# Performance work log

Measured on AMD Instinct MI355X. Metric: run time of the kernel, lower is better.

The kernel has to match this reference:

```python
import math
import jax, jax.numpy as jnp
import numpy as np

B, T, H, A, F = 2, 2048, 2048, 2048, 8192
L, LID, EPS = 24, 0, 1e-5
NEG_INF = -1e38


def setup_inputs() -> dict:
    key = jax.random.key(0)
    ks = jax.random.split(key, 8)
    s = 0.02
    # RWKV init-derived time parameters for layer_id=0, num_hidden_layers=24
    ratio_0_to_1 = LID / (L - 1)          # 0.0
    ratio_1_to_almost_0 = 1.0 - LID / L    # 1.0
    x = jnp.arange(H, dtype=jnp.float32) / H
    tmk = jnp.power(x, ratio_1_to_almost_0)
    tmv = tmk + 0.3 * ratio_0_to_1
    tmr = jnp.power(x, 0.5 * ratio_1_to_almost_0)
    zigzag = 0.5 * (jnp.arange(1, A + 1, dtype=jnp.float32) % 3 - 1)
    time_first = jnp.full((A,), math.log(0.3), dtype=jnp.float32) + zigzag
    h = jnp.arange(A, dtype=jnp.float32)
    time_decay = -5.0 + 8.0 * (h / (A - 1)) ** (0.7 + 1.3 * ratio_0_to_1)
    return {
        'hidden': jax.random.normal(ks[0], (B, T, H), jnp.float32),
        'pre_w': jnp.ones((H,), jnp.float32), 'pre_b': jnp.zeros((H,), jnp.float32),
        'ln1_w': jnp.ones((H,), jnp.float32), 'ln1_b': jnp.zeros((H,), jnp.float32),
        'ln2_w': jnp.ones((H,), jnp.float32), 'ln2_b': jnp.zeros((H,), jnp.float32),
        'time_decay': time_decay, 'time_first': time_first,
        'tmk': tmk, 'tmv': tmv, 'tmr': tmr,
        'Wk': jax.random.normal(ks[1], (H, A), jnp.float32) * s,
        'Wv': jax.random.normal(ks[2], (H, A), jnp.float32) * s,
        'Wr': jax.random.normal(ks[3], (H, A), jnp.float32) * s,
        'Wo': jax.random.normal(ks[4], (A, H), jnp.float32) * s,
        'f_tmk': jnp.power(x, ratio_1_to_almost_0), 'f_tmr': jnp.power(x, ratio_1_to_almost_0),
        'f_Wk': jax.random.normal(ks[5], (H, F), jnp.float32) * s,
        'f_Wr': jax.random.normal(ks[6], (H, H), jnp.float32) * s,
        'f_Wv': jax.random.normal(ks[7], (F, H), jnp.float32) * s,
    }


def _ln(x, w, b):
    mu = x.mean(-1, keepdims=True)
    var = ((x - mu) ** 2).mean(-1, keepdims=True)
    return (x - mu) * jax.lax.rsqrt(var + EPS) * w + b


def _token_shift(x):
    # sx state is zeros at init: prepend a zero row, drop the last token
    return jnp.concatenate((jnp.zeros_like(x[:, :1, :]), x[:, :-1, :]), axis=1)


def _forward(hidden, pre_w, pre_b, ln1_w, ln1_b, ln2_w, ln2_b,
             time_decay, time_first, tmk, tmv, tmr, Wk, Wv, Wr, Wo,
             f_tmk, f_tmr, f_Wk, f_Wr, f_Wv):
    h0 = _ln(hidden, pre_w, pre_b)          # pre_ln (layer_id == 0)
    # ---- time mixing (RwkvSelfAttention) ----
    x1 = _ln(h0, ln1_w, ln1_b)
    cx = _token_shift(x1)
    kx = x1 * tmk + cx * (1 - tmk)
    vx = x1 * tmv + cx * (1 - tmv)
    rx = x1 * tmr + cx * (1 - tmr)
    r = jax.nn.sigmoid(rx @ Wr)             # [B,T,A]
    k = kx @ Wk
    v = vx @ Wv
    w_decay = -jnp.exp(time_decay)          # [A]

    def step(carry, kv):
        aa, bb, pp = carry                  # each [B,A]
        kk, vv = kv                         # each [B,A]
        ww = time_first + kk
        q = jnp.maximum(pp, ww)
        e1 = jnp.exp(pp - q)
        e2 = jnp.exp(ww - q)
        out = (e1 * aa + e2 * vv) / (e1 * bb + e2)
        ww2 = w_decay + pp
        q2 = jnp.maximum(ww2, kk)
        e1 = jnp.exp(ww2 - q2)
        e2 = jnp.exp(kk - q2)
        return (e1 * aa + e2 * vv, e1 * bb + e2, q2), out

    init = (jnp.zeros((B, A), k.dtype), jnp.zeros((B, A), k.dtype),
            jnp.full((B, A), NEG_INF, jnp.float32))
    _, wkv = jax.lax.scan(step, init, (jnp.swapaxes(k, 0, 1), jnp.swapaxes(v, 0, 1)))
    wkv = jnp.swapaxes(wkv, 0, 1)           # [B,T,A]
    h1 = h0 + (r * wkv) @ Wo
    # ---- channel mixing (RwkvFeedForward) ----
    x2 = _ln(h1, ln2_w, ln2_b)
    cx2 = _token_shift(x2)
    kx2 = x2 * f_tmk + cx2 * (1 - f_tmk)
    rx2 = x2 * f_tmr + cx2 * (1 - f_tmr)
    r2 = jax.nn.sigmoid(rx2 @ f_Wr)
    kk2 = jnp.square(jax.nn.relu(kx2 @ f_Wk))
    return h1 + r2 * (kk2 @ f_Wv)


def reference(hidden, pre_w, pre_b, ln1_w, ln1_b, ln2_w, ln2_b,
              time_decay, time_first, tmk, tmv, tmr, Wk, Wv, Wr, Wo,
              f_tmk, f_tmr, f_Wk, f_Wr, f_Wv):
    return _forward(hidden, pre_w, pre_b, ln1_w, ln1_b, ln2_w, ln2_b,
                    time_decay, time_first, tmk, tmv, tmr, Wk, Wv, Wr, Wo,
                    f_tmk, f_tmr, f_Wk, f_Wr, f_Wv)
```

## Files before the change

### kernel.cpp

```cpp
#include <hip/hip_runtime.h>

#define B_  2
#define T_  2048
#define H_  2048
#define A_  2048
#define F_  8192
#define BT_ 4096

typedef __bf16  bf16x8 __attribute__((ext_vector_type(8)));
typedef float   f32x4  __attribute__((ext_vector_type(4)));
typedef short   short8 __attribute__((ext_vector_type(8)));

__device__ __forceinline__ float bf2f(unsigned short b) {
  return __uint_as_float(((unsigned)b) << 16);
}
__device__ __forceinline__ unsigned short f2bf(float f) {
  unsigned u = __float_as_uint(f);
  unsigned r = (u + 0x7FFFu + ((u >> 16) & 1u)) >> 16;
  return (unsigned short)r;
}

typedef __attribute__((address_space(3))) void lds_void_t;
typedef __attribute__((address_space(1))) const void gc_void_t;
__device__ __forceinline__ void gload_lds16(const void* g, void* l) {
  __builtin_amdgcn_global_load_lds((gc_void_t*)g, (lds_void_t*)l, 16, 0, 0);
}

__global__ void canary_kernel(float* out) { out[threadIdx.x] = 1000.0f; }

__global__ __launch_bounds__(256) void transpose5_kernel(
    const float* __restrict__ s0, const float* __restrict__ s1,
    const float* __restrict__ s2, const float* __restrict__ s3,
    const float* __restrict__ s4, unsigned short* __restrict__ dstbase)
{
  __shared__ float tile[32][33];
  const int z = blockIdx.z;
  const float* src = (z == 0) ? s0 : (z == 1) ? s1 : (z == 2) ? s2 : (z == 3) ? s3 : s4;
  unsigned short* dst = dstbase + (size_t)z * 2048 * 2048;
  const int tx = threadIdx.x & 31;
  const int ty = threadIdx.x >> 5;
  const int n0 = blockIdx.x * 32;
  const int k0 = blockIdx.y * 32;
#pragma unroll
  for (int i = 0; i < 32; i += 8)
    tile[ty + i][tx] = src[(size_t)(k0 + ty + i) * 2048 + n0 + tx];
  __syncthreads();
#pragma unroll
  for (int i = 0; i < 32; i += 8)
    dst[(size_t)(n0 + ty + i) * 2048 + k0 + tx] = f2bf(tile[tx][ty + i]);
}

__global__ __launch_bounds__(256) void transpose_bf16_kernel(
    const float* __restrict__ src, unsigned short* __restrict__ dst, int Kd, int Nd)
{
  __shared__ float tile[32][33];
  const int tx = threadIdx.x & 31;
  const int ty = threadIdx.x >> 5;
  const int n0 = blockIdx.x * 32;
  const int k0 = blockIdx.y * 32;
#pragma unroll
  for (int i = 0; i < 32; i += 8)
    tile[ty + i][tx] = src[(size_t)(k0 + ty + i) * Nd + n0 + tx];
  __syncthreads();
#pragma unroll
  for (int i = 0; i < 32; i += 8)
    dst[(size_t)(n0 + ty + i) * Kd + k0 + tx] = f2bf(tile[tx][ty + i]);
}

__device__ __forceinline__ void block_reduce2(float& a, float& b) {
#pragma unroll
  for (int off = 32; off > 0; off >>= 1) {
    a += __shfl_down(a, off, 64);
    b += __shfl_down(b, off, 64);
  }
  __shared__ float sa[4], sb[4];
  const int lane = threadIdx.x & 63, w = threadIdx.x >> 6;
  __syncthreads();
  if (lane == 0) { sa[w] = a; sb[w] = b; }
  __syncthreads();
  a = sa[0] + sa[1] + sa[2] + sa[3];
  b = sb[0] + sb[1] + sb[2] + sb[3];
}

__global__ __launch_bounds__(256) void ln_pre_kernel(
    const float* __restrict__ hidden,
    const float* __restrict__ pw, const float* __restrict__ pb,
    const float* __restrict__ w1, const float* __restrict__ b1,
    float* __restrict__ h0, unsigned short* __restrict__ x1)
{
  const int row = blockIdx.x, tid = threadIdx.x;
  const int c0 = tid * 8;
  const size_t base = (size_t)row * H_ + c0;
  float x[8];
  float4 v0 = *(const float4*)(hidden + base);
  float4 v1 = *(const float4*)(hidden + base + 4);
  x[0]=v0.x; x[1]=v0.y; x[2]=v0.z; x[3]=v0.w;
  x[4]=v1.x; x[5]=v1.y; x[6]=v1.z; x[7]=v1.w;
  float s = 0.f, s2 = 0.f;
#pragma unroll
  for (int j = 0; j < 8; ++j) { s += x[j]; s2 += x[j]*x[j]; }
  block_reduce2(s, s2);
  float mu  = s * (1.f / H_);
  float inv = rsqrtf(fmaxf(s2 * (1.f / H_) - mu*mu, 0.f) + 1e-5f);
  float y[8];
#pragma unroll
  for (int j = 0; j < 8; ++j) y[j] = (x[j] - mu) * inv * pw[c0+j] + pb[c0+j];
  *(float4*)(h0 + base)     = make_float4(y[0],y[1],y[2],y[3]);
  *(float4*)(h0 + base + 4) = make_float4(y[4],y[5],y[6],y[7]);
  s = 0.f; s2 = 0.f;
#pragma unroll
  for (int j = 0; j < 8; ++j) { s += y[j]; s2 += y[j]*y[j]; }
  block_reduce2(s, s2);
  mu  = s * (1.f / H_);
  inv = rsqrtf(fmaxf(s2 * (1.f / H_) - mu*mu, 0.f) + 1e-5f);
  unsigned o[4];
#pragma unroll
  for (int p = 0; p < 4; ++p) {
    unsigned lo = f2bf((y[2*p]   - mu) * inv * w1[c0+2*p]   + b1[c0+2*p]);
    unsigned hi = f2bf((y[2*p+1] - mu) * inv * w1[c0+2*p+1] + b1[c0+2*p+1]);
    o[p] = lo | (hi << 16);
  }
  *(uint4*)(x1 + base) = make_uint4(o[0], o[1], o[2], o[3]);
}

__global__ __launch_bounds__(256) void lnmix2_kernel(
    const float* __restrict__ h1,
    const float* __restrict__ w_, const float* __restrict__ b_,
    const float* __restrict__ tmk_, const float* __restrict__ tmr_,
    unsigned short* __restrict__ kx2b, unsigned short* __restrict__ rx2b)
{
  const int row = blockIdx.x, tid = threadIdx.x;
  const int t = row & (T_ - 1);
  const int c0 = tid * 8;
  const size_t base = (size_t)row * H_ + c0;
  float x[8], p[8];
  {
    float4 v0 = *(const float4*)(h1 + base);
    float4 v1 = *(const float4*)(h1 + base + 4);
    x[0]=v0.x; x[1]=v0.y; x[2]=v0.z; x[3]=v0.w;
    x[4]=v1.x; x[5]=v1.y; x[6]=v1.z; x[7]=v1.w;
  }
  const bool hasp = (t > 0);
  if (hasp) {
    float4 v0 = *(const float4*)(h1 + base - H_);
    float4 v1 = *(const float4*)(h1 + base - H_ + 4);
    p[0]=v0.x; p[1]=v0.y; p[2]=v0.z; p[3]=v0.w;
    p[4]=v1.x; p[5]=v1.y; p[6]=v1.z; p[7]=v1.w;
  } else {
#pragma unroll
    for (int j = 0; j < 8; ++j) p[j] = 0.f;
  }
  float s = 0.f, s2 = 0.f;
#pragma unroll
  for (int j = 0; j < 8; ++j) { s += x[j]; s2 += x[j]*x[j]; }
  block_reduce2(s, s2);
  const float mu  = s * (1.f / H_);
  const float inv = rsqrtf(fmaxf(s2 * (1.f / H_) - mu*mu, 0.f) + 1e-5f);
  float sp = 0.f, sp2 = 0.f;
#pragma unroll
  for (int j = 0; j < 8; ++j) { sp += p[j]; sp2 += p[j]*p[j]; }
  block_reduce2(sp, sp2);
  const float mup  = sp * (1.f / H_);
  const float invp = rsqrtf(fmaxf(sp2 * (1.f / H_) - mup*mup, 0.f) + 1e-5f);
  unsigned ok[4], orr[4];
#pragma unroll
  for (int q = 0; q < 4; ++q) {
    unsigned ko = 0, ro = 0;
#pragma unroll
    for (int h = 0; h < 2; ++h) {
      const int j = q*2 + h;
      const float xr = (x[j] - mu) * inv * w_[c0+j] + b_[c0+j];
      const float cr = hasp ? (p[j] - mup) * invp * w_[c0+j] + b_[c0+j] : 0.f;
      ko |= (unsigned)f2bf(fmaf(xr - cr, tmk_[c0+j], cr)) << (h*16);
      ro |= (unsigned)f2bf(fmaf(xr - cr, tmr_[c0+j], cr)) << (h*16);
    }
    ok[q] = ko; orr[q] = ro;
  }
  *(uint4*)(kx2b + base) = make_uint4(ok[0],ok[1],ok[2],ok[3]);
  *(uint4*)(rx2b + base) = make_uint4(orr[0],orr[1],orr[2],orr[3]);
}

__global__ __launch_bounds__(256) void mix3_kernel(
    const unsigned short* __restrict__ x,
    const float* __restrict__ mk_, const float* __restrict__ mv_, const float* __restrict__ mr_,
    unsigned short* __restrict__ kx, unsigned short* __restrict__ vx, unsigned short* __restrict__ rx)
{
  const int row = blockIdx.x;
  const int t = row & (T_ - 1);
  const int c0 = threadIdx.x * 8;
  const size_t base = (size_t)row * H_ + c0;
  uint4 xv = *(const uint4*)(x + base);
  uint4 cv = make_uint4(0u,0u,0u,0u);
  if (t > 0) cv = *(const uint4*)(x + base - H_);
  const unsigned xs[4] = {xv.x, xv.y, xv.z, xv.w};
  const unsigned cs[4] = {cv.x, cv.y, cv.z, cv.w};
  unsigned ok[4], ov[4], orr[4];
#pragma unroll
  for (int p = 0; p < 4; ++p) {
    unsigned ko=0, vo=0, ro=0;
#pragma unroll
    for (int h = 0; h < 2; ++h) {
      const int j = p*2 + h;
      float xf = bf2f((unsigned short)((xs[p] >> (h*16)) & 0xFFFFu));
      float cf = bf2f((unsigned short)((cs[p] >> (h*16)) & 0xFFFFu));
      float d  = xf - cf;
      ko |= (unsigned)f2bf(fmaf(d, mk_[c0+j], cf)) << (h*16);
      vo |= (unsigned)f2bf(fmaf(d, mv_[c0+j], cf)) << (h*16);
      ro |= (unsigned)f2bf(fmaf(d, mr_[c0+j], cf)) << (h*16);
    }
    ok[p]=ko; ov[p]=vo; orr[p]=ro;
  }
  *(uint4*)(kx + base) = make_uint4(ok[0],ok[1],ok[2],ok[3]);
  *(uint4*)(vx + base) = make_uint4(ov[0],ov[1],ov[2],ov[3]);
  *(uint4*)(rx + base) = make_uint4(orr[0],orr[1],orr[2],orr[3]);
}

#define WKV_G 32
#define WKV_C 32
#define WKV_L 64

__global__ __launch_bounds__(1024) void wkv_scan_kernel(
    const unsigned short* __restrict__ kg, const unsigned short* __restrict__ vg,
    const unsigned short* __restrict__ rg,
    const float* __restrict__ time_first, const float* __restrict__ time_decay,
    unsigned short* __restrict__ rwkv)
{
  const int tid = threadIdx.x;
  const int al  = tid & (WKV_G - 1);
  const int c   = tid >> 5;
  const int b   = blockIdx.x >> 6;
  const int ag  = blockIdx.x & 63;
  const int a   = ag * WKV_G + al;
  const float tf = time_first[a];
  const float w  = -__expf(time_decay[a]);
  const size_t cb = (size_t)b * T_ * A_ + a + (size_t)c * WKV_L * A_;

  float aa = 0.f, bb = 0.f, pp = -1e38f;
  {
    float kb[4], vb[4];
#pragma unroll
    for (int j = 0; j < 4; ++j) {
      kb[j] = bf2f(kg[cb + (size_t)j * A_]);
      vb[j] = bf2f(vg[cb + (size_t)j * A_]);
    }
    for (int t0 = 0; t0 < WKV_L; t0 += 4) {
#pragma unroll
      for (int j = 0; j < 4; ++j) {
        const float kk = kb[j], vv = vb[j];
        const int tn = t0 + j + 4;
        if (tn < WKV_L) {
          kb[j] = bf2f(kg[cb + (size_t)tn * A_]);
          vb[j] = bf2f(vg[cb + (size_t)tn * A_]);
        }
        float ww2 = w + pp;
        float q2  = fmaxf(ww2, kk);
        float e1  = __expf(ww2 - q2);
        float e2  = __expf(kk  - q2);
        aa = e1*aa + e2*vv;
        bb = e1*bb + e2;
        pp = q2;
      }
    }
  }
  __shared__ float saa[WKV_C][WKV_G], sbb[WKV_C][WKV_G], spp[WKV_C][WKV_G];
  saa[c][al] = aa; sbb[c][al] = bb; spp[c][al] = pp;
  __syncthreads();

  if (tid < WKV_G) {
    float Aa = 0.f, Bb = 0.f, Pp = -1e38f;
    const float Lw = (float)WKV_L * w;
    for (int cc = 0; cc < WKV_C; ++cc) {
      const float na = saa[cc][tid], nb = sbb[cc][tid], np = spp[cc][tid];
      saa[cc][tid] = Aa; sbb[cc][tid] = Bb; spp[cc][tid] = Pp;
      const float p1 = Pp + Lw;
      const float pc = fmaxf(p1, np);
      const float f1 = __expf(p1 - pc);
      const float f2 = __expf(np - pc);
      Aa = f1*Aa + f2*na;
      Bb = f1*Bb + f2*nb;
      Pp = pc;
    }
  }
  __syncthreads();
  aa = saa[c][al]; bb = sbb[c][al]; pp = spp[c][al];

  {
    float kb[4], vb[4], rb[4];
#pragma unroll
    for (int j = 0; j < 4; ++j) {
      kb[j] = bf2f(kg[cb + (size_t)j * A_]);
      vb[j] = bf2f(vg[cb + (size_t)j * A_]);
      rb[j] = bf2f(rg[cb + (size_t)j * A_]);
    }
    for (int t0 = 0; t0 < WKV_L; t0 += 4) {
#pragma unroll
      for (int j = 0; j < 4; ++j) {
        const float kk = kb[j], vv = vb[j], rr = rb[j];
        const int tn = t0 + j + 4;
        if (tn < WKV_L) {
          kb[j] = bf2f(kg[cb + (size_t)tn * A_]);
          vb[j] = bf2f(vg[cb + (size_t)tn * A_]);
          rb[j] = bf2f(rg[cb + (size_t)tn * A_]);
        }
        float ww = tf + kk;
        float q  = fmaxf(pp, ww);
        float e1 = __expf(pp - q);
        float e2 = __expf(ww - q);
        float o  = (e1*aa + e2*vv) / (e1*bb + e2);
        float sr = 1.f / (1.f + __expf(-rr));
        rwkv[cb + (size_t)(t0 + j) * A_] = f2bf(sr * o);
        float ww2 = w + pp;
        float q2  = fmaxf(ww2, kk);
        e1 = __expf(ww2 - q2);
        e2 = __expf(kk  - q2);
        aa = e1*aa + e2*vv;
        bb = e1*bb + e2;
        pp = q2;
      }
    }
  }
}

enum { EPI_BF16 = 0, EPI_ADDIP = 1, EPI_RELU2 = 2, EPI_SIGADD = 3 };

template <int BM, int NBUF, int RG, int CG, int EPI>
__global__ __launch_bounds__(512) void gemm4_kernel(
    const unsigned short* __restrict__ Ap, const unsigned short* __restrict__ Bp,
    void* __restrict__ Cp, int K, int Nn,
    const unsigned short* __restrict__ sigb,
    size_t azB, size_t bzB, size_t czB)
{
  constexpr int BN = 256;
  constexpr int FM = BM / 32;
  constexpr int FN = 4;
  __shared__ unsigned short As[NBUF * BM * 64];
  __shared__ unsigned short Bs[NBUF * BN * 64];
  const int zz = blockIdx.z;
  Ap = (const unsigned short*)((const char*)Ap + zz * azB);
  Bp = (const unsigned short*)((const char*)Bp + zz * bzB);
  Cp = (void*)((char*)Cp + zz * czB);
  const int tid  = threadIdx.x;
  const int lane = tid & 63;
  const int lr = lane & 15;
  const int hi = lane >> 4;
  const int rx7 = lr & 7;
  const int wid = tid >> 6;
  const int wm = wid >> 2, wn = wid & 3;
  const int rowW = wm * (BM / 2);
  const int colW = wn * 64;
  const int gx = gridDim.x;
  const int gy = gridDim.y;
  const int flat = blockIdx.y * gx + blockIdx.x;
  const int xcd = flat & 7;
  const int j = flat >> 3;
  const int rgc = gy / RG;
  const int r_idx = xcd % rgc;
  const int c_idx = xcd / rgc;
  const int row_l = j % RG;
  const int col_l = j / RG;
  const long row0 = (long)(r_idx * RG + row_l) * BM;
  const long col0 = (long)(c_idx * CG + col_l) * BN;
  const unsigned short* Ab = Ap + (size_t)row0 * K;
  const unsigned short* Bb = Bp + (size_t)col0 * K;
  const int srow8 = tid >> 3;
  const int sslot = (tid & 7) ^ (srow8 & 7);
  f32x4 acc[FM][FN] = {};

  auto SP0 = [&](int bufi, int tt) {
    unsigned short* asb = As + bufi * (BM * 64);
    unsigned short* bsb = Bs + bufi * (BN * 64);
    const size_t ko = (size_t)tt * 64 + sslot * 8;
    gload_lds16(Ab + (size_t)srow8        * K + ko, asb + tid * 8);
    gload_lds16(Ab + (size_t)(srow8 + 64) * K + ko, asb + 4096 + tid * 8);
    gload_lds16(Bb + (size_t)srow8        * K + ko, bsb + tid * 8);
  };
  auto SP1 = [&](int bufi, int tt) {
    unsigned short* bsb = Bs + bufi * (BN * 64);
    const size_t ko = (size_t)tt * 64 + sslot * 8;
    gload_lds16(Bb + (size_t)(srow8 + 64)  * K + ko, bsb + 4096  + tid * 8);
    gload_lds16(Bb + (size_t)(srow8 + 128) * K + ko, bsb + 8192  + tid * 8);
    gload_lds16(Bb + (size_t)(srow8 + 192) * K + ko, bsb + 12288 + tid * 8);
  };
  auto SPq = [&](int bufi, int tt, int q) {
    const size_t ko = (size_t)tt * 64 + sslot * 8;
    if (q < 2) {
      unsigned short* asb = As + bufi * (BM * 64);
      gload_lds16(Ab + (size_t)(srow8 + q*128)      * K + ko, asb + q*8192 + tid * 8);
      gload_lds16(Ab + (size_t)(srow8 + q*128 + 64) * K + ko, asb + q*8192 + 4096 + tid * 8);
    } else {
      const int qq = q - 2;
      unsigned short* bsb = Bs + bufi * (BN * 64);
      gload_lds16(Bb + (size_t)(srow8 + qq*128)      * K + ko, bsb + qq*8192 + tid * 8);
      gload_lds16(Bb + (size_t)(srow8 + qq*128 + 64) * K + ko, bsb + qq*8192 + 4096 + tid * 8);
    }
  };

  const int nt = K >> 6;
  if constexpr (BM == 128) {
    SP0(0, 0); SP1(0, 0);
    if constexpr (NBUF == 3) { SP0(1, 1); SP1(1, 1); }
  } else {
#pragma unroll
    for (int q = 0; q < 4; ++q) SPq(0, 0, q);
  }
  int cur = 0;
  for (int t = 0; t < nt; ++t) {
    if constexpr (NBUF == 3) {
      if (t + 1 < nt) asm volatile("s_waitcnt vmcnt(6)" ::: "memory");
      else            asm volatile("s_waitcnt vmcnt(0)" ::: "memory");
    } else {
      asm volatile("s_waitcnt vmcnt(0)" ::: "memory");
    }
    __builtin_amdgcn_s_barrier();
    int nb = cur + (NBUF - 1); if (nb >= NBUF) nb -= NBUF;
    const unsigned short* asb = As + cur * (BM * 64);
    const unsigned short* bsb = Bs + cur * (BN * 64);
    if constexpr (BM == 128) {
      bf16x8 af0[4], bf0[4], af1[4], bf1[4];
      const int p0 = (0*4 + hi) ^ rx7;
      const int p1 = (1*4 + hi) ^ rx7;
#pragma unroll
      for (int m = 0; m < 4; ++m)
        af0[m] = __builtin_bit_cast(bf16x8,
            *(const short8*)(asb + (rowW + m*16 + lr) * 64 + p0*8));
#pragma unroll
      for (int n = 0; n < 4; ++n)
        bf0[n] = __builtin_bit_cast(bf16x8,
            *(const short8*)(bsb + (colW + n*16 + lr) * 64 + p0*8));
#pragma unroll
      for (int m = 0; m < 4; ++m)
        af1[m] = __builtin_bit_cast(bf16x8,
            *(const short8*)(asb + (rowW + m*16 + lr) * 64 + p1*8));
#pragma unroll
      for (int n = 0; n < 4; ++n)
        bf1[n] = __builtin_bit_cast(bf16x8,
            *(const short8*)(bsb + (colW + n*16 + lr) * 64 + p1*8));
      if (t + NBUF - 1 < nt) SP0(nb, t + NBUF - 1);
      asm volatile("s_waitcnt lgkmcnt(8)" ::: "memory");
      __builtin_amdgcn_sched_barrier(0);
      __builtin_amdgcn_s_setprio(1);
#pragma unroll
      for (int m = 0; m < 4; ++m)
#pragma unroll
        for (int n = 0; n < 4; ++n)
          acc[m][n] = __builtin_amdgcn_mfma_f32_16x16x32_bf16(af0[m], bf0[n], acc[m][n], 0, 0, 0);
      __builtin_amdgcn_s_setprio(0);
      if (t + NBUF - 1 < nt) SP1(nb, t + NBUF - 1);
      asm volatile("s_waitcnt lgkmcnt(0)" ::: "memory");
      __builtin_amdgcn_sched_barrier(0);
      __builtin_amdgcn_s_setprio(1);
#pragma unroll
      for (int m = 0; m < 4; ++m)
#pragma unroll
        for (int n = 0; n < 4; ++n)
          acc[m][n] = __builtin_amdgcn_mfma_f32_16x16x32_bf16(af1[m], bf1[n], acc[m][n], 0, 0, 0);
      __builtin_amdgcn_s_setprio(0);
    } else {
      bf16x8 aF[2][4], bF[2][4];
      const int p0 = (0*4 + hi) ^ rx7;
      const int p1 = (1*4 + hi) ^ rx7;
#pragma unroll
      for (int n = 0; n < 4; ++n)
        bF[0][n] = __builtin_bit_cast(bf16x8,
            *(const short8*)(bsb + (colW + n*16 + lr) * 64 + p0*8));
#pragma unroll
      for (int m = 0; m < 4; ++m)
        aF[0][m] = __builtin_bit_cast(bf16x8,
            *(const short8*)(asb + (rowW + m*16 + lr) * 64 + p0*8));
#pragma unroll
      for (int m = 0; m < 4; ++m)
        aF[1][m] = __builtin_bit_cast(bf16x8,
            *(const short8*)(asb + (rowW + (4+m)*16 + lr) * 64 + p0*8));
      if (t + 1 < nt) SPq(nb, t + 1, 0);
      asm volatile("s_waitcnt lgkmcnt(4)" ::: "memory");
      __builtin_amdgcn_sched_barrier(0);
      __builtin_amdgcn_s_setprio(1);
#pragma unroll
      for (int m = 0; m < 4; ++m)
#pragma unroll
        for (int n = 0; n < 4; ++n)
          acc[m][n] = __builtin_amdgcn_mfma_f32_16x16x32_bf16(aF[0][m], bF[0][n], acc[m][n], 0, 0, 0);
      __builtin_amdgcn_s_setprio(0);
#pragma unroll
      for (int n = 0; n < 4; ++n)
        bF[1][n] = __builtin_bit_cast(bf16x8,
            *(const short8*)(bsb + (colW + n*16 + lr) * 64 + p1*8));
#pragma unroll
      for (int m = 0; m < 4; ++m)
        aF[0][m] = __builtin_bit_cast(bf16x8,
            *(const short8*)(asb + (rowW + m*16 + lr) * 64 + p1*8));
      if (t + 1 < nt) SPq(nb, t + 1, 1);
      asm volatile("s_waitcnt lgkmcnt(8)" ::: "memory");
      __builtin_amdgcn_sched_barrier(0);
      __builtin_amdgcn_s_setprio(1);
#pragma unroll
      for (int m = 0; m < 4; ++m)
#pragma unroll
        for (int n = 0; n < 4; ++n)
          acc[4+m][n] = __builtin_amdgcn_mfma_f32_16x16x32_bf16(aF[1][m], bF[0][n], acc[4+m][n], 0, 0, 0);
      __builtin_amdgcn_s_setprio(0);
#pragma unroll
      for (int m = 0; m < 4; ++m)
        aF[1][m] = __builtin_bit_cast(bf16x8,
            *(const short8*)(asb + (rowW + (4+m)*16 + lr) * 64 + p1*8));
      if (t + 1 < nt) SPq(nb, t + 1, 2);
      asm volatile("s_waitcnt lgkmcnt(4)" ::: "memory");
      __builtin_amdgcn_sched_barrier(0);
      __builtin_amdgcn_s_setprio(1);
#pragma unroll
      for (int m = 0; m < 4; ++m)
#pragma unroll
        for (int n = 0; n < 4; ++n)
          acc[m][n] = __builtin_amdgcn_mfma_f32_16x16x32_bf16(aF[0][m], bF[1][n], acc[m][n], 0, 0, 0);
      __builtin_amdgcn_s_setprio(0);
      if (t + 1 < nt) SPq(nb, t + 1, 3);
      asm volatile("s_waitcnt lgkmcnt(0)" ::: "memory");
      __builtin_amdgcn_sched_barrier(0);
      __builtin_amdgcn_s_setprio(1);
#pragma unroll
      for (int m = 0; m < 4; ++m)
#pragma unroll
        for (int n = 0; n < 4; ++n)
          acc[4+m][n] = __builtin_amdgcn_mfma_f32_16x16x32_bf16(aF[1][m], bF[1][n], acc[4+m][n], 0, 0, 0);
      __builtin_amdgcn_s_setprio(0);
    }
    cur = (cur + 1 == NBUF) ? 0 : cur + 1;
  }

#pragma unroll
  for (int m = 0; m < FM; ++m) {
#pragma unroll
    for (int n = 0; n < FN; ++n) {
      const long col = col0 + colW + n*16 + lr;
#pragma unroll
      for (int j2 = 0; j2 < 4; ++j2) {
        const long row = row0 + rowW + m*16 + hi*4 + j2;
        const size_t idx = (size_t)row * Nn + col;
        const float v = acc[m][n][j2];
        if (EPI == EPI_BF16) {
          ((unsigned short*)Cp)[idx] = f2bf(v);
        } else if (EPI == EPI_ADDIP) {
          float* C = (float*)Cp;
          C[idx] = C[idx] + v;
        } else if (EPI == EPI_RELU2) {
          float rr = v > 0.f ? v : 0.f;
          ((unsigned short*)Cp)[idx] = f2bf(rr * rr);
        } else {
          float s = 1.f / (1.f + __expf(-bf2f(sigb[idx])));
          float* C = (float*)Cp;
          C[idx] = C[idx] + s * v;
        }
      }
    }
  }
}

#define MB(x) ((size_t)(x) << 20)
#define WS_NEED MB(184)

extern "C" void kernel_launch(void* const* d_in, const int* in_sizes, int n_in,
                              void* d_out, int out_size, void* d_ws, size_t ws_size,
                              hipStream_t stream) {
  const float* hidden     = (const float*)d_in[0];
  const float* pre_w      = (const float*)d_in[1];
  const float* pre_b      = (const float*)d_in[2];
  const float* ln1_w      = (const float*)d_in[3];
  const float* ln1_b      = (const float*)d_in[4];
  const float* ln2_w      = (const float*)d_in[5];
  const float* ln2_b      = (const float*)d_in[6];
  const float* time_decay = (const float*)d_in[7];
  const float* time_first = (const float*)d_in[8];
  const float* tmk        = (const float*)d_in[9];
  const float* tmv        = (const float*)d_in[10];
  const float* tmr        = (const float*)d_in[11];
  const float* Wk         = (const float*)d_in[12];
  const float* Wv         = (const float*)d_in[13];
  const float* Wr         = (const float*)d_in[14];
  const float* Wo         = (const float*)d_in[15];
  const float* f_tmk      = (const float*)d_in[16];
  const float* f_tmr      = (const float*)d_in[17];
  const float* f_Wk       = (const float*)d_in[18];
  const float* f_Wr       = (const float*)d_in[19];
  const float* f_Wv       = (const float*)d_in[20];
  float* out = (float*)d_out;
  char*  ws  = (char*)d_ws;

  if (ws_size < WS_NEED) {
    canary_kernel<<<1, 256, 0, stream>>>(out);
    return;
  }

  unsigned short* MX   = (unsigned short*)(ws + MB(0));
  unsigned short* fWkT = (unsigned short*)(ws + MB(0));
  unsigned short* fWvT = (unsigned short*)(ws + MB(32));
  unsigned short* WkT  = (unsigned short*)(ws + MB(64));
  unsigned short* WoT  = (unsigned short*)(ws + MB(88));
  unsigned short* fWrT = (unsigned short*)(ws + MB(96));
  unsigned short* KK   = (unsigned short*)(ws + MB(64));
  unsigned short* S1   = (unsigned short*)(ws + MB(104));
  unsigned short* kbuf = (unsigned short*)(ws + MB(120));
  unsigned short* vbuf = (unsigned short*)(ws + MB(136));
  unsigned short* rbuf = (unsigned short*)(ws + MB(152));
  unsigned short* M1   = (unsigned short*)(ws + MB(168));

  const dim3 blk(256);
  const dim3 blk512(512);
  const dim3 gSmall(8, 32);
  const dim3 gSmall3(8, 32, 3);
  const dim3 gRelu(32, 16);

  transpose5_kernel<<<dim3(64, 64, 5), blk, 0, stream>>>(Wk, Wv, Wr, Wo, f_Wr, WkT);

  ln_pre_kernel<<<BT_, blk, 0, stream>>>(hidden, pre_w, pre_b, ln1_w, ln1_b, out, S1);

  mix3_kernel<<<BT_, blk, 0, stream>>>(S1, tmk, tmv, tmr, MX, MX + (MB(16)>>1), MX + (MB(32)>>1));
  gemm4_kernel<128,3,8,4,EPI_BF16><<<gSmall3, blk512, 0, stream>>>(
      MX, WkT, kbuf, 2048, 2048, nullptr, MB(16), MB(8), MB(16));

  transpose_bf16_kernel<<<dim3(256, 64), blk, 0, stream>>>(f_Wk, fWkT, 2048, 8192);
  transpose_bf16_kernel<<<dim3(64, 256), blk, 0, stream>>>(f_Wv, fWvT, 8192, 2048);

  wkv_scan_kernel<<<dim3(128), dim3(1024), 0, stream>>>(kbuf, vbuf, rbuf, time_first, time_decay, S1);

  gemm4_kernel<128,3,8,4,EPI_ADDIP><<<gSmall, blk512, 0, stream>>>(
      S1, WoT, out, 2048, 2048, nullptr, 0, 0, 0);

  lnmix2_kernel<<<BT_, blk, 0, stream>>>(out, ln2_w, ln2_b, f_tmk, f_tmr, M1, kbuf);

  gemm4_kernel<128,3,8,4,EPI_BF16><<<gSmall, blk512, 0, stream>>>(
      kbuf, fWrT, vbuf, 2048, 2048, nullptr, 0, 0, 0);

  gemm4_kernel<256,2,8,8,EPI_RELU2><<<gRelu, blk512, 0, stream>>>(
      M1, fWkT, KK, 2048, 8192, nullptr, 0, 0, 0);

  gemm4_kernel<128,3,8,4,EPI_SIGADD><<<gSmall, blk512, 0, stream>>>(
      KK, fWvT, out, 8192, 2048, vbuf, 0, 0, 0);
}
```

Measured before the change: 635.1 us.

## Split-K the final FFN GEMM with larger tiles and a separate sigmoid combine

The K=8192 value GEMM is split into two K=4096 halves, run as a z-batched 256x256-tile GEMM that writes bf16 partial products. A new elementwise kernel sums the partials, applies the sigmoid gate and adds the result into the output. The kvr projection GEMM also moves from 128-row tiles to 256-row tiles with a smaller grid. A leading-dimension parameter is added so GEMMs can address sub-blocks of K. The aim is better tile reuse and occupancy on the long-K GEMM, at the cost of an extra memory pass and bf16 rounding of the partial sums.

```diff
diff --git a/kernel.cpp b/kernel.cpp
--- a/kernel.cpp
+++ b/kernel.cpp
@@ -213,6 +213,35 @@
   *(uint4*)(kx + base) = make_uint4(ok[0],ok[1],ok[2],ok[3]);
   *(uint4*)(vx + base) = make_uint4(ov[0],ov[1],ov[2],ov[3]);
   *(uint4*)(rx + base) = make_uint4(orr[0],orr[1],orr[2],orr[3]);
+}
+
+__global__ __launch_bounds__(256) void sigcombine_kernel(
+    const unsigned short* __restrict__ P0, const unsigned short* __restrict__ P1,
+    const unsigned short* __restrict__ sigb, float* __restrict__ out)
+{
+  const size_t i8 = ((size_t)blockIdx.x * 256 + threadIdx.x) * 8;
+  uint4 a = *(const uint4*)(P0 + i8);
+  uint4 b = *(const uint4*)(P1 + i8);
+  uint4 g = *(const uint4*)(sigb + i8);
+  float4 o0 = *(const float4*)(out + i8);
+  float4 o1 = *(const float4*)(out + i8 + 4);
+  float r[8];
+  const unsigned aw[4] = {a.x,a.y,a.z,a.w};
+  const unsigned bw[4] = {b.x,b.y,b.z,b.w};
+  const unsigned gw[4] = {g.x,g.y,g.z,g.w};
+#pragma unroll
+  for (int p = 0; p < 4; ++p)
+#pragma unroll
+    for (int h = 0; h < 2; ++h) {
+      const float pv = bf2f((unsigned short)((aw[p] >> (h*16)) & 0xFFFFu))
+                     + bf2f((unsigned short)((bw[p] >> (h*16)) & 0xFFFFu));
+      const float sv = 1.f / (1.f + __expf(-bf2f((unsigned short)((gw[p] >> (h*16)) & 0xFFFFu))));
+      r[p*2+h] = sv * pv;
+    }
+  o0.x += r[0]; o0.y += r[1]; o0.z += r[2]; o0.w += r[3];
+  o1.x += r[4]; o1.y += r[5]; o1.z += r[6]; o1.w += r[7];
+  *(float4*)(out + i8)     = o0;
+  *(float4*)(out + i8 + 4) = o1;
 }
 
 #define WKV_G 32
@@ -328,7 +357,7 @@
     const unsigned short* __restrict__ Ap, const unsigned short* __restrict__ Bp,
     void* __restrict__ Cp, int K, int Nn,
     const unsigned short* __restrict__ sigb,
-    size_t azB, size_t bzB, size_t czB)
+    size_t azB, size_t bzB, size_t czB, int lda)
 {
   constexpr int BN = 256;
   constexpr int FM = BM / 32;
@@ -360,8 +389,8 @@
   const int col_l = j / RG;
   const long row0 = (long)(r_idx * RG + row_l) * BM;
   const long col0 = (long)(c_idx * CG + col_l) * BN;
-  const unsigned short* Ab = Ap + (size_t)row0 * K;
-  const unsigned short* Bb = Bp + (size_t)col0 * K;
+  const unsigned short* Ab = Ap + (size_t)row0 * lda;
+  const unsigned short* Bb = Bp + (size_t)col0 * lda;
   const int srow8 = tid >> 3;
   const int sslot = (tid & 7) ^ (srow8 & 7);
   f32x4 acc[FM][FN] = {};
@@ -370,28 +399,28 @@
     unsigned short* asb = As + bufi * (BM * 64);
     unsigned short* bsb = Bs + bufi * (BN * 64);
     const size_t ko = (size_t)tt * 64 + sslot * 8;
-    gload_lds16(Ab + (size_t)srow8        * K + ko, asb + tid * 8);
-    gload_lds16(Ab + (size_t)(srow8 + 64) * K + ko, asb + 4096 + tid * 8);
-    gload_lds16(Bb + (size_t)srow8        * K + ko, bsb + tid * 8);
+    gload_lds16(Ab + (size_t)srow8        * lda + ko, asb + tid * 8);
+    gload_lds16(Ab + (size_t)(srow8 + 64) * lda + ko, asb + 4096 + tid * 8);
+    gload_lds16(Bb + (size_t)srow8        * lda + ko, bsb + tid * 8);
   };
   auto SP1 = [&](int bufi, int tt) {
     unsigned short* bsb = Bs + bufi * (BN * 64);
     const size_t ko = (size_t)tt * 64 + sslot * 8;
-    gload_lds16(Bb + (size_t)(srow8 + 64)  * K + ko, bsb + 4096  + tid * 8);
-    gload_lds16(Bb + (size_t)(srow8 + 128) * K + ko, bsb + 8192  + tid * 8);
-    gload_lds16(Bb + (size_t)(srow8 + 192) * K + ko, bsb + 12288 + tid * 8);
+    gload_lds16(Bb + (size_t)(srow8 + 64)  * lda + ko, bsb + 4096  + tid * 8);
+    gload_lds16(Bb + (size_t)(srow8 + 128) * lda + ko, bsb + 8192  + tid * 8);
+    gload_lds16(Bb + (size_t)(srow8 + 192) * lda + ko, bsb + 12288 + tid * 8);
   };
   auto SPq = [&](int bufi, int tt, int q) {
     const size_t ko = (size_t)tt * 64 + sslot * 8;
     if (q < 2) {
       unsigned short* asb = As + bufi * (BM * 64);
-      gload_lds16(Ab + (size_t)(srow8 + q*128)      * K + ko, asb + q*8192 + tid * 8);
-      gload_lds16(Ab + (size_t)(srow8 + q*128 + 64) * K + ko, asb + q*8192 + 4096 + tid * 8);
+      gload_lds16(Ab + (size_t)(srow8 + q*128)      * lda + ko, asb + q*8192 + tid * 8);
+      gload_lds16(Ab + (size_t)(srow8 + q*128 + 64) * lda + ko, asb + q*8192 + 4096 + tid * 8);
     } else {
       const int qq = q - 2;
       unsigned short* bsb = Bs + bufi * (BN * 64);
-      gload_lds16(Bb + (size_t)(srow8 + qq*128)      * K + ko, bsb + qq*8192 + tid * 8);
-      gload_lds16(Bb + (size_t)(srow8 + qq*128 + 64) * K + ko, bsb + qq*8192 + 4096 + tid * 8);
+      gload_lds16(Bb + (size_t)(srow8 + qq*128)      * lda + ko, bsb + qq*8192 + tid * 8);
+      gload_lds16(Bb + (size_t)(srow8 + qq*128 + 64) * lda + ko, bsb + qq*8192 + 4096 + tid * 8);
     }
   };
 
@@ -602,11 +631,13 @@
   unsigned short* vbuf = (unsigned short*)(ws + MB(136));
   unsigned short* rbuf = (unsigned short*)(ws + MB(152));
   unsigned short* M1   = (unsigned short*)(ws + MB(168));
+  unsigned short* PK   = (unsigned short*)(ws + MB(152));
 
   const dim3 blk(256);
   const dim3 blk512(512);
   const dim3 gSmall(8, 32);
-  const dim3 gSmall3(8, 32, 3);
+  const dim3 gBig3(8, 16, 3);
+  const dim3 gBig2(8, 16, 2);
   const dim3 gRelu(32, 16);
 
   transpose5_kernel<<<dim3(64, 64, 5), blk, 0, stream>>>(Wk, Wv, Wr, Wo, f_Wr, WkT);
@@ -614,8 +645,8 @@
   ln_pre_kernel<<<BT_, blk, 0, stream>>>(hidden, pre_w, pre_b, ln1_w, ln1_b, out, S1);
 
   mix3_kernel<<<BT_, blk, 0, stream>>>(S1, tmk, tmv, tmr, MX, MX + (MB(16)>>1), MX + (MB(32)>>1));
-  gemm4_kernel<128,3,8,4,EPI_BF16><<<gSmall3, blk512, 0, stream>>>(
-      MX, WkT, kbuf, 2048, 2048, nullptr, MB(16), MB(8), MB(16));
+  gemm4_kernel<256,2,8,2,EPI_BF16><<<gBig3, blk512, 0, stream>>>(
+      MX, WkT, kbuf, 2048, 2048, nullptr, MB(16), MB(8), MB(16), 2048);
 
   transpose_bf16_kernel<<<dim3(256, 64), blk, 0, stream>>>(f_Wk, fWkT, 2048, 8192);
   transpose_bf16_kernel<<<dim3(64, 256), blk, 0, stream>>>(f_Wv, fWvT, 8192, 2048);
@@ -623,16 +654,18 @@
   wkv_scan_kernel<<<dim3(128), dim3(1024), 0, stream>>>(kbuf, vbuf, rbuf, time_first, time_decay, S1);
 
   gemm4_kernel<128,3,8,4,EPI_ADDIP><<<gSmall, blk512, 0, stream>>>(
-      S1, WoT, out, 2048, 2048, nullptr, 0, 0, 0);
+      S1, WoT, out, 2048, 2048, nullptr, 0, 0, 0, 2048);
 
   lnmix2_kernel<<<BT_, blk, 0, stream>>>(out, ln2_w, ln2_b, f_tmk, f_tmr, M1, kbuf);
 
   gemm4_kernel<128,3,8,4,EPI_BF16><<<gSmall, blk512, 0, stream>>>(
-      kbuf, fWrT, vbuf, 2048, 2048, nullptr, 0, 0, 0);
+      kbuf, fWrT, vbuf, 2048, 2048, nullptr, 0, 0, 0, 2048);
 
   gemm4_kernel<256,2,8,8,EPI_RELU2><<<gRelu, blk512, 0, stream>>>(
-      M1, fWkT, KK, 2048, 8192, nullptr, 0, 0, 0);
-
-  gemm4_kernel<128,3,8,4,EPI_SIGADD><<<gSmall, blk512, 0, stream>>>(
-      KK, fWvT, out, 8192, 2048, vbuf, 0, 0, 0);
-}
+      M1, fWkT, KK, 2048, 8192, nullptr, 0, 0, 0, 2048);
+
+  gemm4_kernel<256,2,8,2,EPI_BF16><<<gBig2, blk512, 0, stream>>>(
+      KK, fWvT, PK, 4096, 2048, nullptr, (size_t)4096*2, (size_t)4096*2, MB(16), 8192);
+
+  sigcombine_kernel<<<dim3(4096), blk, 0, stream>>>(PK, PK + (MB(16)>>1), vbuf, out);
+}
```

New measurement: 643.6 us. About the same (+1.3%).
